# Kernel tuning notes

Hardware: AMD Instinct MI355X
Metric: run time of the kernel (lower is better)

The kernel has to match this reference:

```python
import jax, jax.numpy as jnp
import numpy as np

N = 100000      # nodes
E = 1600000     # edges (avg degree 16)
F_IN = 15       # num_features from source
H1, H2, OUT = 64, 32, 2
BN_EPS = 1e-5


def _lin(key, out_dim, in_dim):
    return (jax.random.normal(key, (out_dim, in_dim), dtype=jnp.float32)
            * np.float32(1.0 / np.sqrt(in_dim)))


def setup_inputs() -> dict:
    key = jax.random.key(0)
    ks = jax.random.split(key, 16)
    x = jax.random.normal(ks[0], (N, F_IN), dtype=jnp.float32)
    edge_index = jax.random.randint(ks[1], (2, E), 0, N)
    return {
        "x": x,
        "edge_index": edge_index,
        # SAGEConv layer 1 (lin_l on aggregated neighbors w/ bias, lin_r on root no bias)
        "W1l": _lin(ks[2], H1, F_IN), "b1l": jnp.zeros((H1,), jnp.float32),
        "W1r": _lin(ks[3], H1, F_IN),
        "g1": jnp.ones((H1,), jnp.float32), "beta1": jnp.zeros((H1,), jnp.float32),
        # SAGEConv layer 2
        "W2l": _lin(ks[4], H2, H1), "b2l": jnp.zeros((H2,), jnp.float32),
        "W2r": _lin(ks[5], H2, H1),
        "g2": jnp.ones((H2,), jnp.float32), "beta2": jnp.zeros((H2,), jnp.float32),
        # SAGEConv layer 3
        "W3l": _lin(ks[6], OUT, H2), "b3l": jnp.zeros((OUT,), jnp.float32),
        "W3r": _lin(ks[7], OUT, H2),
    }


def sage_conv(x, src, dst, Wl, bl, Wr, n):
    # mean-aggregate neighbor features x[src] at dst, then linear + root linear
    msg = x[src]                                           # [E, d]
    agg = jax.ops.segment_sum(msg, dst, num_segments=n)    # [N, d]
    deg = jax.ops.segment_sum(jnp.ones((src.shape[0],), x.dtype), dst,
                              num_segments=n)              # [N]
    mean = agg / jnp.maximum(deg, 1.0)[:, None]
    return mean @ Wl.T + bl + x @ Wr.T


def batch_norm(x, gamma, beta):
    mu = x.mean(axis=0)
    var = x.var(axis=0)  # biased, as torch BN uses for normalization
    return (x - mu) * jax.lax.rsqrt(var + BN_EPS) * gamma + beta


def reference(x, edge_index, W1l, b1l, W1r, g1, beta1,
              W2l, b2l, W2r, g2, beta2, W3l, b3l, W3r):
    src, dst = edge_index[0], edge_index[1]
    n = x.shape[0]
    h = sage_conv(x, src, dst, W1l, b1l, W1r, n)
    h = jax.nn.relu(batch_norm(h, g1, beta1))
    h = sage_conv(h, src, dst, W2l, b2l, W2r, n)
    h = jax.nn.relu(batch_norm(h, g2, beta2))
    h = sage_conv(h, src, dst, W3l, b3l, W3r, n)
    return jax.nn.log_softmax(h, axis=1)
```

## Files before the change

### kernel.cpp

```cpp
#include <hip/hip_runtime.h>
#include <hip/hip_bf16.h>
#include <math.h>

#define N_NODES 100000
#define N_EDGES 1600000
#define F_IN 15
#define H1 64
#define H2 32
#define BN_EPS 1e-5f
#define NBLK 2048
#define RELU1(v) fmaxf(fmaf((v), scale, shift), 0.f)

__device__ __forceinline__ unsigned short f2bf(float f) {
    unsigned u = __float_as_uint(f);
    u += 0x7FFFu + ((u >> 16) & 1u);
    return (unsigned short)(u >> 16);
}
__device__ __forceinline__ float bf2f(unsigned short h) {
    return __uint_as_float(((unsigned)h) << 16);
}
__device__ __forceinline__ float bcast(float v, int k) {
    return __int_as_float(__builtin_amdgcn_readlane(__float_as_int(v), k));
}


__global__ void k_deg(const int* __restrict__ dst, int* __restrict__ deg) {
    int e = blockIdx.x * blockDim.x + threadIdx.x;
    if (e < N_EDGES) atomicAdd(&deg[dst[e]], 1);
}

__global__ void k_scan_a(const int* __restrict__ deg, int* __restrict__ off,
                         int* __restrict__ part) {
    __shared__ int s[1024];
    int i = blockIdx.x * 1024 + threadIdx.x;
    int v = (i < N_NODES) ? deg[i] : 0;
    s[threadIdx.x] = v;
    __syncthreads();
    for (int o = 1; o < 1024; o <<= 1) {
        int t = (threadIdx.x >= o) ? s[threadIdx.x - o] : 0;
        __syncthreads();
        s[threadIdx.x] += t;
        __syncthreads();
    }
    if (i < N_NODES) off[i] = s[threadIdx.x] - v;
    if (threadIdx.x == 1023) part[blockIdx.x] = s[1023];
}

__global__ void k_scan_b(int* __restrict__ part, int nb) {
    __shared__ int s[128];
    int v = (threadIdx.x < nb) ? part[threadIdx.x] : 0;
    s[threadIdx.x] = v;
    __syncthreads();
    for (int o = 1; o < 128; o <<= 1) {
        int t = (threadIdx.x >= o) ? s[threadIdx.x - o] : 0;
        __syncthreads();
        s[threadIdx.x] += t;
        __syncthreads();
    }
    if (threadIdx.x < nb) part[threadIdx.x] = s[threadIdx.x] - v;
}

__global__ void k_scan_c(int* __restrict__ off, int* __restrict__ cur,
                         const int* __restrict__ part) {
    int i = blockIdx.x * blockDim.x + threadIdx.x;
    if (i < N_NODES) {
        int v = off[i] + part[i >> 10];
        off[i] = v;
        cur[i] = v;
    }
    if (i == 0) off[N_NODES] = N_EDGES;
}

__global__ void k_fill(const int* __restrict__ src, const int* __restrict__ dst,
                       int* __restrict__ cur, int* __restrict__ srt) {
    int e = blockIdx.x * blockDim.x + threadIdx.x;
    if (e < N_EDGES) {
        int p = atomicAdd(&cur[dst[e]], 1);
        srt[p] = src[e];
    }
}


__launch_bounds__(256)
__global__ void k_l1(const float* __restrict__ x, const int* __restrict__ off,
                     const int* __restrict__ srt,
                     const float* __restrict__ W1l, const float* __restrict__ b1l,
                     const float* __restrict__ W1r,
                     unsigned short* __restrict__ h1b, float* __restrict__ stats) {
    __shared__ float m_lds[4][16], o_lds[4][16];
    __shared__ float sred[2 * H1];
    int lane = threadIdx.x & 63;
    int h4 = lane >> 4;
    int k  = lane & 15;
    int w = threadIdx.x >> 6;
    int gw = blockIdx.x * 4 + w;
    const int NW = NBLK * 4;

    float wl[F_IN], wr[F_IN];
#pragma unroll
    for (int kk = 0; kk < F_IN; ++kk) {
        wl[kk] = W1l[lane * F_IN + kk];
        wr[kk] = W1r[lane * F_IN + kk];
    }
    float bj = b1l[lane];

    if (threadIdx.x < 2 * H1) sred[threadIdx.x] = 0.f;
    __syncthreads();

    float sS = 0.f, sQ = 0.f;
    for (int n = gw; n < N_NODES; n += NW) {
        int o0 = off[n], o1 = off[n + 1];
        float sum = 0.f;
        int i = o0;
        for (; i + 16 <= o1; i += 16) {
            int my = (lane < 16) ? srt[i + lane] : 0;
            float v[4];
#pragma unroll
            for (int b = 0; b < 4; ++b) {
                int s = __shfl(my, b * 4 + h4, 64);
                v[b] = (k < F_IN) ? x[(long)s * F_IN + k] : 0.f;
            }
            sum += (v[0] + v[1]) + (v[2] + v[3]);
        }
        for (; i < o1; ++i) {
            int s = srt[i];
            if (lane < F_IN) sum += x[(long)s * F_IN + lane];
        }
        sum += __shfl_xor(sum, 16, 64);
        sum += __shfl_xor(sum, 32, 64);
        float inv = 1.f / (float)max(o1 - o0, 1);
        if (lane < F_IN) {
            m_lds[w][lane] = sum * inv;
            o_lds[w][lane] = x[(long)n * F_IN + lane];
        }
        float acc = bj;
#pragma unroll
        for (int kk = 0; kk < F_IN; ++kk)
            acc += m_lds[w][kk] * wl[kk] + o_lds[w][kk] * wr[kk];
        h1b[(long)n * H1 + lane] = f2bf(acc);
        sS += acc; sQ += acc * acc;
    }
    atomicAdd(&sred[lane], sS);
    atomicAdd(&sred[H1 + lane], sQ);
    __syncthreads();
    if (threadIdx.x < 2 * H1) atomicAdd(&stats[threadIdx.x], sred[threadIdx.x]);
}


__launch_bounds__(256, 2)
__global__ void k_t2(const unsigned short* __restrict__ h1b,
                     const float* __restrict__ W2l, const float* __restrict__ b2l,
                     const float* __restrict__ W2r,
                     const float* __restrict__ g1, const float* __restrict__ beta1,
                     const float* __restrict__ stats1,
                     unsigned short* __restrict__ t2b, float* __restrict__ r2) {
    int lane = threadIdx.x & 63;
    int w = threadIdx.x >> 6;
    int gw = blockIdx.x * 4 + w;
    const int NW = NBLK * 4;

    float mu = stats1[lane] * (1.f / N_NODES);
    float var = stats1[H1 + lane] * (1.f / N_NODES) - mu * mu;
    float scale = rsqrtf(var + BN_EPS) * g1[lane];
    float shift = beta1[lane] - mu * scale;

    const float* wsrc = (lane < H2) ? (W2l + lane * H1) : (W2r + (lane - H2) * H1);
    float wreg[H1];
#pragma unroll
    for (int kk = 0; kk < H1; ++kk) wreg[kk] = wsrc[kk];
    float addc = (lane < H2) ? 0.f : b2l[lane - H2];

    for (int n = gw; n < N_NODES; n += NW) {
        float y = RELU1(bf2f(h1b[(long)n * H1 + lane]));
        float acc = addc;
#pragma unroll
        for (int kk = 0; kk < H1; ++kk)
            acc = fmaf(bcast(y, kk), wreg[kk], acc);
        if (lane < H2) t2b[(long)n * H2 + lane] = f2bf(acc);
        else           r2[(long)n * H2 + (lane - H2)] = acc;
    }
}


__launch_bounds__(256)
__global__ void k_a2(const unsigned short* __restrict__ t2b, const float* __restrict__ r2,
                     const int* __restrict__ off, const int* __restrict__ srt,
                     float* __restrict__ h2p, float* __restrict__ stats2) {
    __shared__ float sred[2 * H2];
    int lane = threadIdx.x & 63;
    int j = lane & 31;
    int h = lane >> 5;
    int w = threadIdx.x >> 6;
    int gw = blockIdx.x * 4 + w;
    const int NW = NBLK * 4;

    if (threadIdx.x < 2 * H2) sred[threadIdx.x] = 0.f;
    __syncthreads();

    float sS = 0.f, sQ = 0.f;
    for (int n = gw; n < N_NODES; n += NW) {
        int o0 = off[n], o1 = off[n + 1];
        float sum = 0.f;
        int i = o0;
        for (; i + 16 <= o1; i += 16) {
            int my = (lane < 16) ? srt[i + lane] : 0;
            float v[8];
#pragma unroll
            for (int b = 0; b < 8; ++b) {
                int s0 = __shfl(my, 2 * b, 64);
                int s1 = __shfl(my, 2 * b + 1, 64);
                int s = h ? s1 : s0;
                v[b] = bf2f(t2b[(long)s * H2 + j]);
            }
            sum += (((v[0]+v[1])+(v[2]+v[3])) + ((v[4]+v[5])+(v[6]+v[7])));
        }
        for (; i + 2 <= o1; i += 2) {
            int s0 = srt[i], s1 = srt[i + 1];
            int s = h ? s1 : s0;
            sum += bf2f(t2b[(long)s * H2 + j]);
        }
        if (i < o1) {
            int s = srt[i];
            if (!h) sum += bf2f(t2b[(long)s * H2 + j]);
        }
        sum += __shfl_xor(sum, 32, 64);
        float inv = 1.f / (float)max(o1 - o0, 1);
        if (lane < H2) {
            float hp = fmaf(sum, inv, r2[(long)n * H2 + j]);
            h2p[(long)n * H2 + j] = hp;
            sS += hp; sQ += hp * hp;
        }
    }
    if (lane < H2) {
        atomicAdd(&sred[j], sS);
        atomicAdd(&sred[H2 + j], sQ);
    }
    __syncthreads();
    if (threadIdx.x < 2 * H2) atomicAdd(&stats2[threadIdx.x], sred[threadIdx.x]);
}


__launch_bounds__(256)
__global__ void k_t3(const float* __restrict__ h2p,
                     const float* __restrict__ W3l, const float* __restrict__ b3l,
                     const float* __restrict__ W3r,
                     const float* __restrict__ g2, const float* __restrict__ beta2,
                     const float* __restrict__ stats2,
                     float* __restrict__ t3, float* __restrict__ r3) {
    int lane = threadIdx.x & 63;
    int j = lane & 31;
    int h = lane >> 5;
    int w = threadIdx.x >> 6;
    int gw = blockIdx.x * 4 + w;
    const int NW = NBLK * 4;

    float mu = stats2[j] * (1.f / N_NODES);
    float var = stats2[H2 + j] * (1.f / N_NODES) - mu * mu;
    float scale = rsqrtf(var + BN_EPS) * g2[j];
    float shift = beta2[j] - mu * scale;

    float wl0 = W3l[j], wl1 = W3l[H2 + j];
    float wr0 = W3r[j], wr1 = W3r[H2 + j];
    float b0 = b3l[0], b1 = b3l[1];

    for (int p = gw; p < N_NODES / 2; p += NW) {
        int n = p * 2 + h;
        float y = RELU1(h2p[(long)n * H2 + j]);
        float p0 = y * wl0, p1 = y * wl1, q0 = y * wr0, q1 = y * wr1;
#pragma unroll
        for (int s = 16; s > 0; s >>= 1) {
            p0 += __shfl_xor(p0, s, 32);
            p1 += __shfl_xor(p1, s, 32);
            q0 += __shfl_xor(q0, s, 32);
            q1 += __shfl_xor(q1, s, 32);
        }
        if (j == 0) {
            *(float2*)(t3 + (long)n * 2) = make_float2(p0, p1);
            *(float2*)(r3 + (long)n * 2) = make_float2(q0 + b0, q1 + b1);
        }
    }
}


__launch_bounds__(256)
__global__ void k_a3(const float* __restrict__ t3, const float* __restrict__ r3,
                     const int* __restrict__ off, const int* __restrict__ srt,
                     float* __restrict__ out) {
    int n = blockIdx.x * 256 + threadIdx.x;
    if (n >= N_NODES) return;
    int o0 = off[n], o1 = off[n + 1];
    float s0 = 0.f, s1 = 0.f;
    int i = o0;
    for (; i + 8 <= o1; i += 8) {
        int sidx[8];
#pragma unroll
        for (int b = 0; b < 8; ++b) sidx[b] = srt[i + b];
        float2 v[8];
#pragma unroll
        for (int b = 0; b < 8; ++b) v[b] = *(const float2*)(t3 + (long)sidx[b] * 2);
#pragma unroll
        for (int b = 0; b < 8; ++b) { s0 += v[b].x; s1 += v[b].y; }
    }
    for (; i < o1; ++i) {
        float2 v = *(const float2*)(t3 + (long)srt[i] * 2);
        s0 += v.x; s1 += v.y;
    }
    float inv = 1.f / (float)max(o1 - o0, 1);
    float2 rr = *(const float2*)(r3 + (long)n * 2);
    float z0 = fmaf(s0, inv, rr.x);
    float z1 = fmaf(s1, inv, rr.y);
    float m = fmaxf(z0, z1);
    float l = m + logf(__expf(z0 - m) + __expf(z1 - m));
    out[(long)n * 2 + 0] = z0 - l;
    out[(long)n * 2 + 1] = z1 - l;
}


extern "C" void kernel_launch(void* const* d_in, const int* in_sizes, int n_in,
                              void* d_out, int out_size, void* d_ws, size_t ws_size,
                              hipStream_t stream) {
    const float* x    = (const float*)d_in[0];
    const int*   ei   = (const int*)d_in[1];
    const float* W1l  = (const float*)d_in[2];
    const float* b1l  = (const float*)d_in[3];
    const float* W1r  = (const float*)d_in[4];
    const float* g1   = (const float*)d_in[5];
    const float* bt1  = (const float*)d_in[6];
    const float* W2l  = (const float*)d_in[7];
    const float* b2l  = (const float*)d_in[8];
    const float* W2r  = (const float*)d_in[9];
    const float* g2   = (const float*)d_in[10];
    const float* bt2  = (const float*)d_in[11];
    const float* W3l  = (const float*)d_in[12];
    const float* b3l  = (const float*)d_in[13];
    const float* W3r  = (const float*)d_in[14];
    float* out = (float*)d_out;

    float* stats1 = (float*)d_ws;
    float* stats2 = stats1 + 128;
    int* deg  = (int*)d_ws + 256;
    int* off  = deg + 100096;
    int* cur  = off + 100096;
    int* srt  = cur + 100096;
    int* part = srt + 1600000;
    unsigned short* h1b = (unsigned short*)(part + 256);
    float* h2p = (float*)h1b;
    unsigned short* t2b = (unsigned short*)((int*)(part + 256) + 3200000);
    float* r2 = (float*)((int*)(part + 256) + 3200000 + 1600000);
    float* t3 = r2 + 3200000;
    float* r3 = t3 + 200000;

    const int* srcv = ei;
    const int* dstv = ei + N_EDGES;

    hipMemsetAsync(d_ws, 0, (256 + 100096) * sizeof(int), stream);

    k_deg   <<<(N_EDGES + 255) / 256, 256, 0, stream>>>(dstv, deg);
    k_scan_a<<<98, 1024, 0, stream>>>(deg, off, part);
    k_scan_b<<<1, 128, 0, stream>>>(part, 98);
    k_scan_c<<<(N_NODES + 255) / 256, 256, 0, stream>>>(off, cur, part);
    k_fill  <<<(N_EDGES + 255) / 256, 256, 0, stream>>>(srcv, dstv, cur, srt);
    k_l1    <<<NBLK, 256, 0, stream>>>(x, off, srt, W1l, b1l, W1r, h1b, stats1);
    k_t2    <<<NBLK, 256, 0, stream>>>(h1b, W2l, b2l, W2r, g1, bt1, stats1, t2b, r2);
    k_a2    <<<NBLK, 256, 0, stream>>>(t2b, r2, off, srt, h2p, stats2);
    k_t3    <<<NBLK, 256, 0, stream>>>(h2p, W3l, b3l, W3r, g2, bt2, stats2, t3, r3);
    k_a3    <<<(N_NODES + 255) / 256, 256, 0, stream>>>(t3, r3, off, srt, out);
}
```

Baseline: 588.3 us.

## Pad CSR segments to multiples of four with sentinel entries to simplify gather tails

Each node's CSR segment is rounded up to a multiple of four slots. The padding slots are filled with -1 via a memset, so aggregation loops can process edges in groups of 4 with a sentinel check instead of scalar tail loops. Degree now comes from the deg array rather than the offset difference. In k_l1 and k_a2 the shuffle-based index broadcast is replaced by direct per-lane srt loads. This adds a memset of about 7.6 MB, more srt traffic, and extra predication per load.

```diff
diff --git a/kernel.cpp b/kernel.cpp
--- a/kernel.cpp
+++ b/kernel.cpp
@@ -9,6 +9,7 @@
 #define H2 32
 #define BN_EPS 1e-5f
 #define NBLK 2048
+#define SRT_CAP 1900032
 #define RELU1(v) fmaxf(fmaf((v), scale, shift), 0.f)
 
 __device__ __forceinline__ unsigned short f2bf(float f) {
@@ -33,7 +34,8 @@
                          int* __restrict__ part) {
     __shared__ int s[1024];
     int i = blockIdx.x * 1024 + threadIdx.x;
-    int v = (i < N_NODES) ? deg[i] : 0;
+    int d = (i < N_NODES) ? deg[i] : 0;
+    int v = (d + 3) & ~3;
     s[threadIdx.x] = v;
     __syncthreads();
     for (int o = 1; o < 1024; o <<= 1) {
@@ -61,14 +63,14 @@
 }
 
 __global__ void k_scan_c(int* __restrict__ off, int* __restrict__ cur,
-                         const int* __restrict__ part) {
+                         const int* __restrict__ part, const int* __restrict__ deg) {
     int i = blockIdx.x * blockDim.x + threadIdx.x;
     if (i < N_NODES) {
         int v = off[i] + part[i >> 10];
         off[i] = v;
         cur[i] = v;
-    }
-    if (i == 0) off[N_NODES] = N_EDGES;
+        if (i == N_NODES - 1) off[N_NODES] = v + ((deg[i] + 3) & ~3);
+    }
 }
 
 __global__ void k_fill(const int* __restrict__ src, const int* __restrict__ dst,
@@ -83,7 +85,7 @@
 
 __launch_bounds__(256)
 __global__ void k_l1(const float* __restrict__ x, const int* __restrict__ off,
-                     const int* __restrict__ srt,
+                     const int* __restrict__ srt, const int* __restrict__ deg,
                      const float* __restrict__ W1l, const float* __restrict__ b1l,
                      const float* __restrict__ W1r,
                      unsigned short* __restrict__ h1b, float* __restrict__ stats) {
@@ -110,25 +112,25 @@
     float sS = 0.f, sQ = 0.f;
     for (int n = gw; n < N_NODES; n += NW) {
         int o0 = off[n], o1 = off[n + 1];
+        int dg = deg[n];
         float sum = 0.f;
         int i = o0;
         for (; i + 16 <= o1; i += 16) {
-            int my = (lane < 16) ? srt[i + lane] : 0;
-            float v[4];
-#pragma unroll
-            for (int b = 0; b < 4; ++b) {
-                int s = __shfl(my, b * 4 + h4, 64);
-                v[b] = (k < F_IN) ? x[(long)s * F_IN + k] : 0.f;
-            }
-            sum += (v[0] + v[1]) + (v[2] + v[3]);
-        }
-        for (; i < o1; ++i) {
-            int s = srt[i];
-            if (lane < F_IN) sum += x[(long)s * F_IN + lane];
+            int s0 = srt[i + h4], s1 = srt[i + 4 + h4],
+                s2 = srt[i + 8 + h4], s3 = srt[i + 12 + h4];
+            float v0 = (s0 >= 0 && k < F_IN) ? x[(long)s0 * F_IN + k] : 0.f;
+            float v1 = (s1 >= 0 && k < F_IN) ? x[(long)s1 * F_IN + k] : 0.f;
+            float v2 = (s2 >= 0 && k < F_IN) ? x[(long)s2 * F_IN + k] : 0.f;
+            float v3 = (s3 >= 0 && k < F_IN) ? x[(long)s3 * F_IN + k] : 0.f;
+            sum += (v0 + v1) + (v2 + v3);
+        }
+        for (; i < o1; i += 4) {
+            int s = srt[i + h4];
+            sum += (s >= 0 && k < F_IN) ? x[(long)s * F_IN + k] : 0.f;
         }
         sum += __shfl_xor(sum, 16, 64);
         sum += __shfl_xor(sum, 32, 64);
-        float inv = 1.f / (float)max(o1 - o0, 1);
+        float inv = 1.f / (float)max(dg, 1);
         if (lane < F_IN) {
             m_lds[w][lane] = sum * inv;
             o_lds[w][lane] = x[(long)n * F_IN + lane];
@@ -185,6 +187,7 @@
 __launch_bounds__(256)
 __global__ void k_a2(const unsigned short* __restrict__ t2b, const float* __restrict__ r2,
                      const int* __restrict__ off, const int* __restrict__ srt,
+                     const int* __restrict__ deg,
                      float* __restrict__ h2p, float* __restrict__ stats2) {
     __shared__ float sred[2 * H2];
     int lane = threadIdx.x & 63;
@@ -200,31 +203,26 @@
     float sS = 0.f, sQ = 0.f;
     for (int n = gw; n < N_NODES; n += NW) {
         int o0 = off[n], o1 = off[n + 1];
+        int dg = deg[n];
         float sum = 0.f;
         int i = o0;
         for (; i + 16 <= o1; i += 16) {
-            int my = (lane < 16) ? srt[i + lane] : 0;
             float v[8];
 #pragma unroll
             for (int b = 0; b < 8; ++b) {
-                int s0 = __shfl(my, 2 * b, 64);
-                int s1 = __shfl(my, 2 * b + 1, 64);
-                int s = h ? s1 : s0;
-                v[b] = bf2f(t2b[(long)s * H2 + j]);
+                int s = srt[i + 2 * b + h];
+                v[b] = (s >= 0) ? bf2f(t2b[(long)s * H2 + j]) : 0.f;
             }
             sum += (((v[0]+v[1])+(v[2]+v[3])) + ((v[4]+v[5])+(v[6]+v[7])));
         }
-        for (; i + 2 <= o1; i += 2) {
-            int s0 = srt[i], s1 = srt[i + 1];
-            int s = h ? s1 : s0;
-            sum += bf2f(t2b[(long)s * H2 + j]);
-        }
-        if (i < o1) {
-            int s = srt[i];
-            if (!h) sum += bf2f(t2b[(long)s * H2 + j]);
+        for (; i < o1; i += 4) {
+            int s0 = srt[i + h], s1 = srt[i + 2 + h];
+            float u0 = (s0 >= 0) ? bf2f(t2b[(long)s0 * H2 + j]) : 0.f;
+            float u1 = (s1 >= 0) ? bf2f(t2b[(long)s1 * H2 + j]) : 0.f;
+            sum += u0 + u1;
         }
         sum += __shfl_xor(sum, 32, 64);
-        float inv = 1.f / (float)max(o1 - o0, 1);
+        float inv = 1.f / (float)max(dg, 1);
         if (lane < H2) {
             float hp = fmaf(sum, inv, r2[(long)n * H2 + j]);
             h2p[(long)n * H2 + j] = hp;
@@ -285,27 +283,38 @@
 __launch_bounds__(256)
 __global__ void k_a3(const float* __restrict__ t3, const float* __restrict__ r3,
                      const int* __restrict__ off, const int* __restrict__ srt,
-                     float* __restrict__ out) {
+                     const int* __restrict__ deg, float* __restrict__ out) {
     int n = blockIdx.x * 256 + threadIdx.x;
     if (n >= N_NODES) return;
     int o0 = off[n], o1 = off[n + 1];
+    int dg = deg[n];
     float s0 = 0.f, s1 = 0.f;
     int i = o0;
     for (; i + 8 <= o1; i += 8) {
-        int sidx[8];
-#pragma unroll
-        for (int b = 0; b < 8; ++b) sidx[b] = srt[i + b];
-        float2 v[8];
-#pragma unroll
-        for (int b = 0; b < 8; ++b) v[b] = *(const float2*)(t3 + (long)sidx[b] * 2);
-#pragma unroll
-        for (int b = 0; b < 8; ++b) { s0 += v[b].x; s1 += v[b].y; }
-    }
-    for (; i < o1; ++i) {
-        float2 v = *(const float2*)(t3 + (long)srt[i] * 2);
-        s0 += v.x; s1 += v.y;
-    }
-    float inv = 1.f / (float)max(o1 - o0, 1);
+        int sx[8];
+#pragma unroll
+        for (int b = 0; b < 8; ++b) sx[b] = srt[i + b];
+#pragma unroll
+        for (int b = 0; b < 8; ++b) {
+            if (sx[b] >= 0) {
+                float2 v = *(const float2*)(t3 + (long)sx[b] * 2);
+                s0 += v.x; s1 += v.y;
+            }
+        }
+    }
+    for (; i < o1; i += 4) {
+        int sx[4];
+#pragma unroll
+        for (int b = 0; b < 4; ++b) sx[b] = srt[i + b];
+#pragma unroll
+        for (int b = 0; b < 4; ++b) {
+            if (sx[b] >= 0) {
+                float2 v = *(const float2*)(t3 + (long)sx[b] * 2);
+                s0 += v.x; s1 += v.y;
+            }
+        }
+    }
+    float inv = 1.f / (float)max(dg, 1);
     float2 rr = *(const float2*)(r3 + (long)n * 2);
     float z0 = fmaf(s0, inv, rr.x);
     float z1 = fmaf(s1, inv, rr.y);
@@ -342,7 +351,7 @@
     int* off  = deg + 100096;
     int* cur  = off + 100096;
     int* srt  = cur + 100096;
-    int* part = srt + 1600000;
+    int* part = srt + SRT_CAP;
     unsigned short* h1b = (unsigned short*)(part + 256);
     float* h2p = (float*)h1b;
     unsigned short* t2b = (unsigned short*)((int*)(part + 256) + 3200000);
@@ -354,15 +363,16 @@
     const int* dstv = ei + N_EDGES;
 
     hipMemsetAsync(d_ws, 0, (256 + 100096) * sizeof(int), stream);
+    hipMemsetAsync(srt, 0xFF, (size_t)SRT_CAP * sizeof(int), stream);
 
     k_deg   <<<(N_EDGES + 255) / 256, 256, 0, stream>>>(dstv, deg);
     k_scan_a<<<98, 1024, 0, stream>>>(deg, off, part);
     k_scan_b<<<1, 128, 0, stream>>>(part, 98);
-    k_scan_c<<<(N_NODES + 255) / 256, 256, 0, stream>>>(off, cur, part);
+    k_scan_c<<<(N_NODES + 255) / 256, 256, 0, stream>>>(off, cur, part, deg);
     k_fill  <<<(N_EDGES + 255) / 256, 256, 0, stream>>>(srcv, dstv, cur, srt);
-    k_l1    <<<NBLK, 256, 0, stream>>>(x, off, srt, W1l, b1l, W1r, h1b, stats1);
+    k_l1    <<<NBLK, 256, 0, stream>>>(x, off, srt, deg, W1l, b1l, W1r, h1b, stats1);
     k_t2    <<<NBLK, 256, 0, stream>>>(h1b, W2l, b2l, W2r, g1, bt1, stats1, t2b, r2);
-    k_a2    <<<NBLK, 256, 0, stream>>>(t2b, r2, off, srt, h2p, stats2);
+    k_a2    <<<NBLK, 256, 0, stream>>>(t2b, r2, off, srt, deg, h2p, stats2);
     k_t3    <<<NBLK, 256, 0, stream>>>(h2p, W3l, b3l, W3r, g2, bt2, stats2, t3, r3);
-    k_a3    <<<(N_NODES + 255) / 256, 256, 0, stream>>>(t3, r3, off, srt, out);
-}
+    k_a3    <<<(N_NODES + 255) / 256, 256, 0, stream>>>(t3, r3, off, srt, deg, out);
+}
```

Result: faster. 570.0 us (-3.1%).
